# Kernel optimization log

Hardware: AMD Instinct MI355X
Metric: run time of the kernel (lower is better)

Reference implementation:

```python
import jax, jax.numpy as jnp
import numpy as np

B, S, D, H = 4, 2048, 256, 8
SPARSITY = 0.1


def setup_inputs() -> dict:
    key = jax.random.key(0)
    ks = jax.random.split(key, 6)
    s = 0.02
    return {
        "x": jax.random.normal(ks[0], (B, S, D), jnp.float32),
        # nn.MultiheadAttention packed in-projection (W_q;W_k;W_v) and out-projection
        "w_in": jax.random.normal(ks[1], (3 * D, D), jnp.float32) * s,
        "b_in": jnp.zeros((3 * D,), jnp.float32),
        "w_out": jax.random.normal(ks[2], (D, D), jnp.float32) * s,
        "b_out": jnp.zeros((D,), jnp.float32),
        # sparsity gate: Linear(D, D//4) -> ReLU -> Linear(D//4, 1) -> Sigmoid
        "gate_w1": jax.random.normal(ks[3], (D // 4, D), jnp.float32) * s,
        "gate_b1": jnp.zeros((D // 4,), jnp.float32),
        "gate_w2": jax.random.normal(ks[4], (1, D // 4), jnp.float32) * s,
        "gate_b2": jnp.zeros((1,), jnp.float32),
    }


def reference(x, w_in, b_in, w_out, b_out, gate_w1, gate_b1, gate_w2, gate_b2):
    b, s, d = x.shape
    hd = d // H

    # --- adaptive sparse mask (top-k importance gating) ---
    h = jax.nn.relu(jnp.einsum('bsd,fd->bsf', x, gate_w1) + gate_b1)
    importance = jax.nn.sigmoid(jnp.einsum('bsf,of->bso', h, gate_w2) + gate_b2)[..., 0]  # [B,S]
    k = max(1, int(s * SPARSITY))
    _, top_idx = jax.lax.top_k(importance, k)  # [B,k]
    keep = jnp.zeros((b, s), dtype=bool).at[jnp.arange(b)[:, None], top_idx].set(True)  # [B,S]

    # --- multi-head attention with key_padding_mask = ~keep ---
    qkv = jnp.einsum('bsd,ed->bse', x, w_in) + b_in  # [B,S,3D]
    q, kk, v = jnp.split(qkv, 3, axis=-1)
    split_heads = lambda t: t.reshape(b, s, H, hd).transpose(0, 2, 1, 3)  # [B,H,S,hd]
    q, kk, v = split_heads(q), split_heads(kk), split_heads(v)

    scores = jnp.einsum('bhqd,bhkd->bhqk', q, kk) / jnp.sqrt(jnp.asarray(hd, x.dtype))
    neg = jnp.finfo(scores.dtype).min
    scores = jnp.where(keep[:, None, None, :], scores, neg)  # mask non-selected keys
    attn = jax.nn.softmax(scores, axis=-1)

    out = jnp.einsum('bhqk,bhkd->bhqd', attn, v)
    out = out.transpose(0, 2, 1, 3).reshape(b, s, d)
    return jnp.einsum('bsd,od->bso', out, w_out) + b_out
```

## Files before the change

### kernel.cpp

```cpp
#include <hip/hip_runtime.h>
#include <hip/hip_bf16.h>

#define B_  4
#define S_  2048
#define D_  256
#define H_  8
#define HD_ 32
#define K_  204
#define SCALE_ 0.17677669529663687f

#define OFF_IMP    0
#define OFF_KG     8192
#define OFF_VG     217088
#define OFF_FLAGS  425984
#define OFF_KIDX   434176
#define OFF_Q      435200
#define OFF_AO     2532352

typedef __attribute__((ext_vector_type(8))) short short8v;
typedef __attribute__((ext_vector_type(4))) float f32x4;

static __device__ __forceinline__ unsigned short f2bf(float f) {
    unsigned int u = __float_as_uint(f);
    u += 0x7FFFu + ((u >> 16) & 1u);
    return (unsigned short)(u >> 16);
}
static __device__ __forceinline__ float bf2f(unsigned short h) {
    return __uint_as_float((unsigned int)h << 16);
}
static __device__ __forceinline__ short8v pack_bf8(float4 a, float4 b) {
    short8v r;
    r[0]=(short)f2bf(a.x); r[1]=(short)f2bf(a.y); r[2]=(short)f2bf(a.z); r[3]=(short)f2bf(a.w);
    r[4]=(short)f2bf(b.x); r[5]=(short)f2bf(b.y); r[6]=(short)f2bf(b.z); r[7]=(short)f2bf(b.w);
    return r;
}
static __device__ __forceinline__ short8v ld_bf8(const unsigned short* p) {
    union { unsigned int u[4]; short8v v; } cv;
    const uint2 a  = *(const uint2*)(p);
    const uint2 b2 = *(const uint2*)(p + 4);
    cv.u[0] = a.x; cv.u[1] = a.y; cv.u[2] = b2.x; cv.u[3] = b2.y;
    return cv.v;
}
static __device__ __forceinline__ void cvt_store16(
    unsigned short* hi, unsigned short* lo, const float4* v)
{
    #pragma unroll
    for (int q = 0; q < 2; ++q) {
        short8v h, l;
        #pragma unroll
        for (int e = 0; e < 2; ++e) {
            const float4 f = v[q*2 + e];
            const unsigned short h0 = f2bf(f.x), h1 = f2bf(f.y),
                                 h2 = f2bf(f.z), h3 = f2bf(f.w);
            h[e*4+0]=(short)h0; h[e*4+1]=(short)h1; h[e*4+2]=(short)h2; h[e*4+3]=(short)h3;
            l[e*4+0]=(short)f2bf(f.x - bf2f(h0));
            l[e*4+1]=(short)f2bf(f.y - bf2f(h1));
            l[e*4+2]=(short)f2bf(f.z - bf2f(h2));
            l[e*4+3]=(short)f2bf(f.w - bf2f(h3));
        }
        *(short8v*)(hi + q*8) = h;
        *(short8v*)(lo + q*8) = l;
    }
}

__global__ __launch_bounds__(256) void gate_kernel(
    const float* __restrict__ x, const float* __restrict__ gw1,
    const float* __restrict__ gb1, const float* __restrict__ gw2, float* ws)
{
    const int t0 = blockIdx.x * 8;
    const int tid = threadIdx.x;
    __shared__ __align__(16) float xs[8 * D_];
    __shared__ float hred[8 * 64];

    const float4* src = (const float4*)(x + (size_t)t0 * D_);
    ((float4*)xs)[tid]       = src[tid];
    ((float4*)xs)[tid + 256] = src[tid + 256];
    __syncthreads();

    const int c = tid & 3, f = tid >> 2;
    float4 wv[16];
    const float4* wr = (const float4*)(gw1 + (size_t)f * D_) + c;
    #pragma unroll
    for (int j = 0; j < 16; ++j) wv[j] = wr[j * 4];
    const float bb = gb1[f], g2 = gw2[f];

    #pragma unroll
    for (int tk = 0; tk < 8; ++tk) {
        const float4* xr = (const float4*)(xs + tk * D_) + c;
        float a = 0.0f;
        #pragma unroll
        for (int j = 0; j < 16; ++j) {
            float4 xv = xr[j * 4];
            a += wv[j].x*xv.x + wv[j].y*xv.y + wv[j].z*xv.z + wv[j].w*xv.w;
        }
        a += __shfl_xor(a, 1);
        a += __shfl_xor(a, 2);
        if (c == 0) hred[tk * 64 + f] = fmaxf(a + bb, 0.0f) * g2;
    }
    __syncthreads();

    const int tk = tid >> 5, ln = tid & 31;
    float s = hred[tk * 64 + ln] + hred[tk * 64 + ln + 32];
    #pragma unroll
    for (int o = 16; o; o >>= 1) s += __shfl_xor(s, o, 32);
    if (ln == 0) ws[OFF_IMP + t0 + tk] = s;
}

__global__ __launch_bounds__(256) void rank_kernel(const float* __restrict__ ws_imp, int* flags)
{
    const int b  = blockIdx.x >> 7;
    const int ic = blockIdx.x & 127;
    const int tid = threadIdx.x;
    __shared__ __align__(16) float vs[S_];
    const float* src = ws_imp + b * S_;
    #pragma unroll
    for (int cc = 0; cc < S_/(256*4); ++cc)
        ((float4*)vs)[tid + cc*256] = ((const float4*)src)[tid + cc*256];
    __syncthreads();

    const int il = tid >> 4;
    const int c  = tid & 15;
    const int i  = ic * 16 + il;
    const float vi = vs[i];
    int gt = 0, eq = 0;
    const float4* v4 = (const float4*)vs + c * 32;
    #pragma unroll 8
    for (int t = 0; t < 32; ++t) {
        const int j4 = (t + c) & 31;
        float4 w = v4[j4];
        const int base = c * 128 + j4 * 4;
        gt += (w.x > vi); eq += (w.x == vi) && (base + 0 < i);
        gt += (w.y > vi); eq += (w.y == vi) && (base + 1 < i);
        gt += (w.z > vi); eq += (w.z == vi) && (base + 2 < i);
        gt += (w.w > vi); eq += (w.w == vi) && (base + 3 < i);
    }
    int r = gt + eq;
    r += __shfl_xor(r, 1);
    r += __shfl_xor(r, 2);
    r += __shfl_xor(r, 4);
    r += __shfl_xor(r, 8);
    if (c == 0) flags[b * S_ + i] = (r < K_) ? 1 : 0;
}

__global__ __launch_bounds__(256) void emit_kernel(const int* __restrict__ flags, int* kidx)
{
    const int b = blockIdx.x;
    const int t = threadIdx.x;
    __shared__ int fl[S_];
    __shared__ int cs[256];
    const int* src = flags + b * S_;
    #pragma unroll
    for (int c = 0; c < S_/256; ++c) fl[t + c*256] = src[t + c*256];
    __syncthreads();

    int s = 0;
    #pragma unroll
    for (int c = 0; c < 8; ++c) s += fl[t*8 + c];
    cs[t] = s;
    __syncthreads();
    for (int off = 1; off < 256; off <<= 1) {
        int v = (t >= off) ? cs[t - off] : 0;
        __syncthreads();
        cs[t] += v;
        __syncthreads();
    }
    int pos = cs[t] - s;
    #pragma unroll
    for (int c = 0; c < 8; ++c) {
        int idx = t*8 + c;
        if (fl[idx]) { if (pos < K_) kidx[b * K_ + pos] = idx; ++pos; }
    }
}

__global__ __launch_bounds__(256) void kv_kernel(
    const float* __restrict__ x, const float* __restrict__ w_in,
    const float* __restrict__ b_in, float* ws, const int* __restrict__ kidx)
{
    const int b = blockIdx.y, j0 = blockIdx.x * 4, tid = threadIdx.x;
    __shared__ __align__(16) float xs[4 * D_];
    __shared__ int toks[4];
    if (tid < 4) {
        int tk = kidx[b * K_ + j0 + tid];
        toks[tid] = min(max(tk, 0), S_ - 1);
    }
    __syncthreads();
    {
        const int kk = tid >> 6, l = tid & 63;
        ((float4*)xs)[kk * 64 + l] =
            ((const float4*)(x + ((size_t)b * S_ + toks[kk]) * D_))[l];
    }
    __syncthreads();

    const int c = tid & 3, f = tid >> 2;
    #pragma unroll 1
    for (int fg = 0; fg < 8; ++fg) {
        const int eh = fg * 64 + f;
        float4 wv[16];
        const float4* wr = (const float4*)(w_in + (size_t)(D_ + eh) * D_) + c;
        #pragma unroll
        for (int j = 0; j < 16; ++j) wv[j] = wr[j * 4];
        float a0 = 0, a1 = 0, a2 = 0, a3 = 0;
        #pragma unroll
        for (int j = 0; j < 16; ++j) {
            float4 w = wv[j];
            float4 x0 = ((const float4*)(xs + 0*D_))[c + j*4];
            float4 x1 = ((const float4*)(xs + 1*D_))[c + j*4];
            float4 x2 = ((const float4*)(xs + 2*D_))[c + j*4];
            float4 x3 = ((const float4*)(xs + 3*D_))[c + j*4];
            a0 += w.x*x0.x + w.y*x0.y + w.z*x0.z + w.w*x0.w;
            a1 += w.x*x1.x + w.y*x1.y + w.z*x1.z + w.w*x1.w;
            a2 += w.x*x2.x + w.y*x2.y + w.z*x2.z + w.w*x2.w;
            a3 += w.x*x3.x + w.y*x3.y + w.z*x3.z + w.w*x3.w;
        }
        a0 += __shfl_xor(a0, 1); a0 += __shfl_xor(a0, 2);
        a1 += __shfl_xor(a1, 1); a1 += __shfl_xor(a1, 2);
        a2 += __shfl_xor(a2, 1); a2 += __shfl_xor(a2, 2);
        a3 += __shfl_xor(a3, 1); a3 += __shfl_xor(a3, 2);
        if (c == 0) {
            const float bias = b_in[D_ + eh];
            const int isV = eh >> 8;
            const int ee = eh & 255;
            const int h = ee >> 5, d = ee & 31;
            float* dst = ws + (isV ? OFF_VG : OFF_KG) + ((b * H_ + h) * K_) * HD_ + d;
            dst[(j0 + 0) * HD_] = a0 + bias;
            dst[(j0 + 1) * HD_] = a1 + bias;
            dst[(j0 + 2) * HD_] = a2 + bias;
            dst[(j0 + 3) * HD_] = a3 + bias;
        }
    }
}

#define GSTR 80

__global__ __launch_bounds__(256) void gemm_kernel(
    const float* __restrict__ A, const float* __restrict__ W,
    const float* __restrict__ bias, float* __restrict__ C)
{
    __shared__ __align__(16) unsigned short Ash[64 * GSTR];
    __shared__ __align__(16) unsigned short Asl[64 * GSTR];
    __shared__ __align__(16) unsigned short Bsh[64 * GSTR];
    __shared__ __align__(16) unsigned short Bsl[64 * GSTR];

    const int tid = threadIdx.x;
    const int m0 = blockIdx.x * 64, n0 = blockIdx.y * 64;
    const int lane = tid & 63, w = tid >> 6;
    const int c = lane & 15, g = lane >> 4;
    const int mq = w >> 1, nq = w & 1;

    const f32x4 zf = {0.0f, 0.0f, 0.0f, 0.0f};
    f32x4 acc[2][2] = {{zf, zf}, {zf, zf}};

    const int srow = tid >> 2, sseg = tid & 3;
    const float* Ap = A + (size_t)(m0 + srow) * D_ + sseg * 16;
    const float* Wp = W + (size_t)(n0 + srow) * D_ + sseg * 16;

    float4 ar[4], br[4];
    #pragma unroll
    for (int j = 0; j < 4; ++j) { ar[j] = ((const float4*)Ap)[j]; br[j] = ((const float4*)Wp)[j]; }

    for (int k0 = 0; k0 < D_; k0 += 64) {
        __syncthreads();
        cvt_store16(&Ash[srow*GSTR + sseg*16], &Asl[srow*GSTR + sseg*16], ar);
        cvt_store16(&Bsh[srow*GSTR + sseg*16], &Bsl[srow*GSTR + sseg*16], br);
        __syncthreads();
        if (k0 + 64 < D_) {
            #pragma unroll
            for (int j = 0; j < 4; ++j) {
                ar[j] = ((const float4*)(Ap + k0 + 64))[j];
                br[j] = ((const float4*)(Wp + k0 + 64))[j];
            }
        }
        #pragma unroll
        for (int ks = 0; ks < 2; ++ks) {
            short8v am[2][2], bm[2][2];
            #pragma unroll
            for (int t = 0; t < 2; ++t) {
                const int ra = (mq*32 + t*16 + c) * GSTR + ks*32 + g*8;
                am[t][0] = *(const short8v*)&Ash[ra];
                am[t][1] = *(const short8v*)&Asl[ra];
                const int rb = (nq*32 + t*16 + c) * GSTR + ks*32 + g*8;
                bm[t][0] = *(const short8v*)&Bsh[rb];
                bm[t][1] = *(const short8v*)&Bsl[rb];
            }
            #pragma unroll
            for (int mt = 0; mt < 2; ++mt)
                #pragma unroll
                for (int nt = 0; nt < 2; ++nt) {
                    acc[mt][nt] = __builtin_amdgcn_mfma_f32_16x16x32_bf16(am[mt][0], bm[nt][0], acc[mt][nt], 0, 0, 0);
                    acc[mt][nt] = __builtin_amdgcn_mfma_f32_16x16x32_bf16(am[mt][0], bm[nt][1], acc[mt][nt], 0, 0, 0);
                    acc[mt][nt] = __builtin_amdgcn_mfma_f32_16x16x32_bf16(am[mt][1], bm[nt][0], acc[mt][nt], 0, 0, 0);
                }
        }
    }
    #pragma unroll
    for (int nt = 0; nt < 2; ++nt) {
        const int n = n0 + nq*32 + nt*16 + c;
        const float bv = bias[n];
        #pragma unroll
        for (int mt = 0; mt < 2; ++mt) {
            const int m = m0 + mq*32 + mt*16 + g*4;
            #pragma unroll
            for (int r = 0; r < 4; ++r)
                C[(size_t)(m + r) * D_ + n] = acc[mt][nt][r] + bv;
        }
    }
}

#define PSTR 228
#define VSTR 228

__global__ __launch_bounds__(256) void attn_kernel(const float* __restrict__ ws, float* __restrict__ ao)
{
    const int b = blockIdx.z, h = blockIdx.y, q0 = blockIdx.x * 32;
    const int tid = threadIdx.x;
    const int lane = tid & 63, w = tid >> 6;
    const int c = lane & 15, g = lane >> 4;

    __shared__ __align__(16) unsigned short Pl[32 * PSTR];
    __shared__ __align__(16) unsigned short VTl[32 * VSTR];
    __shared__ float redl[4 * 32];
    __shared__ float invl[32];

    const float* KGb = ws + OFF_KG + (size_t)(b * H_ + h) * K_ * HD_;
    const float* VGb = ws + OFF_VG + (size_t)(b * H_ + h) * K_ * HD_;

    for (int i = tid; i < K_ * 8; i += 256) {
        const int j = i >> 3, dc = i & 7;
        const float4 v = ((const float4*)VGb)[i];
        VTl[(dc*4+0)*VSTR + j] = f2bf(v.x);
        VTl[(dc*4+1)*VSTR + j] = f2bf(v.y);
        VTl[(dc*4+2)*VSTR + j] = f2bf(v.z);
        VTl[(dc*4+3)*VSTR + j] = f2bf(v.w);
    }
    {
        const int q = tid >> 3, cc = tid & 7;
        *(unsigned int*)&Pl[q * PSTR + 208 + cc * 2] = 0u;
    }
    for (int i = tid; i < 32 * 20; i += 256) {
        VTl[(i / 20) * VSTR + 204 + (i % 20)] = 0;
    }

    short8v qa[2];
    #pragma unroll
    for (int qt = 0; qt < 2; ++qt) {
        const float* qp = ws + OFF_Q + (size_t)(b * S_ + q0 + qt*16 + c) * D_ + h * HD_ + g * 8;
        qa[qt] = pack_bf8(*(const float4*)qp, *(const float4*)(qp + 4));
    }
    const int njt = (w == 0) ? 4 : 3;
    f32x4 acc[2][4];
    const f32x4 zf = {0.0f, 0.0f, 0.0f, 0.0f};
    #pragma unroll
    for (int qt = 0; qt < 2; ++qt)
        #pragma unroll
        for (int t = 0; t < 4; ++t) acc[qt][t] = zf;

    for (int t = 0; t < njt; ++t) {
        const int jt = w + 4 * t;
        const int jc = min(jt * 16 + c, K_ - 1);
        const float* kp = KGb + (size_t)jc * HD_ + g * 8;
        const short8v kb = pack_bf8(*(const float4*)kp, *(const float4*)(kp + 4));
        acc[0][t] = __builtin_amdgcn_mfma_f32_16x16x32_bf16(qa[0], kb, acc[0][t], 0, 0, 0);
        acc[1][t] = __builtin_amdgcn_mfma_f32_16x16x32_bf16(qa[1], kb, acc[1][t], 0, 0, 0);
    }

    float rs[2][4] = {{0,0,0,0},{0,0,0,0}};
    for (int t = 0; t < njt; ++t) {
        const int jg = (w + 4 * t) * 16 + c;
        const bool val = (jg < K_);
        #pragma unroll
        for (int qt = 0; qt < 2; ++qt) {
            #pragma unroll
            for (int r = 0; r < 4; ++r) {
                const float e = val ? __expf(acc[qt][t][r] * SCALE_) : 0.0f;
                rs[qt][r] += e;
                Pl[(qt*16 + g*4 + r) * PSTR + jg] = f2bf(e);
            }
        }
    }
    #pragma unroll
    for (int qt = 0; qt < 2; ++qt)
        #pragma unroll
        for (int r = 0; r < 4; ++r) {
            float s = rs[qt][r];
            s += __shfl_xor(s, 1); s += __shfl_xor(s, 2);
            s += __shfl_xor(s, 4); s += __shfl_xor(s, 8);
            if (c == 0) redl[w * 32 + qt*16 + g*4 + r] = s;
        }

    __syncthreads();
    if (tid < 32)
        invl[tid] = 1.0f / (redl[tid] + redl[32 + tid] + redl[64 + tid] + redl[96 + tid]);
    __syncthreads();

    const int dt = w >> 1, qt2 = w & 1;
    f32x4 o = zf;
    const unsigned short* vb = &VTl[(dt*16 + c) * VSTR];
    const unsigned short* pb = &Pl[(qt2*16 + c) * PSTR];
    #pragma unroll
    for (int kt = 0; kt < 7; ++kt) {
        const short8v av = ld_bf8(vb + kt*32 + g*8);
        const short8v bv = ld_bf8(pb + kt*32 + g*8);
        o = __builtin_amdgcn_mfma_f32_16x16x32_bf16(av, bv, o, 0, 0, 0);
    }
    const float iv = invl[qt2*16 + c];
    float4 r4; r4.x = o[0]*iv; r4.y = o[1]*iv; r4.z = o[2]*iv; r4.w = o[3]*iv;
    *(float4*)(ao + (size_t)(b * S_ + q0 + qt2*16 + c) * D_ + h * HD_ + dt*16 + g*4) = r4;
}

extern "C" void kernel_launch(void* const* d_in, const int* in_sizes, int n_in,
                              void* d_out, int out_size, void* d_ws, size_t ws_size,
                              hipStream_t stream)
{
    const float* x     = (const float*)d_in[0];
    const float* w_in  = (const float*)d_in[1];
    const float* b_in  = (const float*)d_in[2];
    const float* w_out = (const float*)d_in[3];
    const float* b_out = (const float*)d_in[4];
    const float* gw1   = (const float*)d_in[5];
    const float* gb1   = (const float*)d_in[6];
    const float* gw2   = (const float*)d_in[7];

    float* ws = (float*)d_ws;
    int* flags = (int*)(ws + OFF_FLAGS);
    int* kidx  = (int*)(ws + OFF_KIDX);
    float* out = (float*)d_out;

    gate_kernel<<<B_ * S_ / 8, 256, 0, stream>>>(x, gw1, gb1, gw2, ws);
    rank_kernel<<<B_ * 128, 256, 0, stream>>>(ws + OFF_IMP, flags);
    emit_kernel<<<B_, 256, 0, stream>>>(flags, kidx);
    kv_kernel<<<dim3(51, B_), 256, 0, stream>>>(x, w_in, b_in, ws, kidx);
    gemm_kernel<<<dim3(B_ * S_ / 64, D_ / 64), 256, 0, stream>>>(x, w_in, b_in, ws + OFF_Q);
    attn_kernel<<<dim3(S_ / 32, H_, B_), 256, 0, stream>>>(ws, ws + OFF_AO);
    gemm_kernel<<<dim3(B_ * S_ / 64, D_ / 64), 256, 0, stream>>>(ws + OFF_AO, w_out, b_out, out);
}
```

Before: 167.3 us.

## Fuse all stages into a persistent megakernel with grid-wide barriers

Replaces the seven separate launches with one persistent kernel of 512 blocks. Each block walks virtual tiles of every stage (gate, Q projection, rank, K/V gather projection, attention, output projection), and atomic-counter grid barriers separate the dependent stages, with shared memory reused through a union. The separate emit/prefix-scan pass is dropped: rank now appends selected indices through an atomic counter, so key order is nondeterministic. The goal is to remove per-launch gaps and to overlap the gate and Q GEMM, at the cost of spin-barrier overhead and a deadlock risk if all 512 blocks are not co-resident.

```diff
diff --git a/kernel.cpp b/kernel.cpp
--- a/kernel.cpp
+++ b/kernel.cpp
@@ -12,10 +12,14 @@
 #define OFF_IMP    0
 #define OFF_KG     8192
 #define OFF_VG     217088
-#define OFF_FLAGS  425984
+#define OFF_META   425984
 #define OFF_KIDX   434176
 #define OFF_Q      435200
 #define OFF_AO     2532352
+
+#define GSTR 80
+#define PSTR 228
+#define VSTR 228
 
 typedef __attribute__((ext_vector_type(8))) short short8v;
 typedef __attribute__((ext_vector_type(4))) float f32x4;
@@ -63,14 +67,44 @@
     }
 }
 
-__global__ __launch_bounds__(256) void gate_kernel(
-    const float* __restrict__ x, const float* __restrict__ gw1,
-    const float* __restrict__ gb1, const float* __restrict__ gw2, float* ws)
-{
-    const int t0 = blockIdx.x * 8;
+struct SharedU {
+    union {
+        struct { float xs[8 * D_]; float hred[8 * 64]; } g;
+        struct { float vs[S_]; } r;
+        struct { float xs[4 * D_]; int toks[4]; } k;
+        struct { unsigned short Ash[64*GSTR]; unsigned short Asl[64*GSTR];
+                 unsigned short Bsh[64*GSTR]; unsigned short Bsl[64*GSTR]; } m;
+        struct { unsigned short Pl[32*PSTR]; unsigned short VTl[32*VSTR];
+                 float redl[4*32]; float invl[32]; } a;
+    };
+};
+
+static __device__ __forceinline__ void grid_barrier(int* meta, int target)
+{
+    __syncthreads();
+    if (threadIdx.x == 0) {
+        __threadfence();
+        if (atomicAdd(&meta[0], 1) == (int)gridDim.x - 1) {
+            atomicExch(&meta[0], 0);
+            __threadfence();
+            atomicAdd(&meta[1], 1);
+        } else {
+            while (atomicAdd(&meta[1], 0) < target) __builtin_amdgcn_s_sleep(2);
+        }
+        __threadfence();
+    }
+    __syncthreads();
+}
+
+static __device__ __forceinline__ void gate_tile(
+    SharedU& sh, const float* __restrict__ x, const float* __restrict__ gw1,
+    const float* __restrict__ gb1, const float* __restrict__ gw2, float* ws, int vt)
+{
+    const int t0 = vt * 8;
     const int tid = threadIdx.x;
-    __shared__ __align__(16) float xs[8 * D_];
-    __shared__ float hred[8 * 64];
+    float* xs = sh.g.xs;
+    float* hred = sh.g.hred;
+    __syncthreads();
 
     const float4* src = (const float4*)(x + (size_t)t0 * D_);
     ((float4*)xs)[tid]       = src[tid];
@@ -106,15 +140,17 @@
     if (ln == 0) ws[OFF_IMP + t0 + tk] = s;
 }
 
-__global__ __launch_bounds__(256) void rank_kernel(const float* __restrict__ ws_imp, int* flags)
-{
-    const int b  = blockIdx.x >> 7;
-    const int ic = blockIdx.x & 127;
+static __device__ __forceinline__ void rank_tile(
+    SharedU& sh, const float* __restrict__ imp, int* kidx, int* meta, int vt)
+{
+    const int b  = vt >> 7;
+    const int ic = vt & 127;
     const int tid = threadIdx.x;
-    __shared__ __align__(16) float vs[S_];
-    const float* src = ws_imp + b * S_;
-    #pragma unroll
-    for (int cc = 0; cc < S_/(256*4); ++cc)
+    float* vs = sh.r.vs;
+    __syncthreads();
+    const float* src = imp + b * S_;
+    #pragma unroll
+    for (int cc = 0; cc < 2; ++cc)
         ((float4*)vs)[tid + cc*256] = ((const float4*)src)[tid + cc*256];
     __syncthreads();
 
@@ -139,46 +175,21 @@
     r += __shfl_xor(r, 2);
     r += __shfl_xor(r, 4);
     r += __shfl_xor(r, 8);
-    if (c == 0) flags[b * S_ + i] = (r < K_) ? 1 : 0;
-}
-
-__global__ __launch_bounds__(256) void emit_kernel(const int* __restrict__ flags, int* kidx)
-{
-    const int b = blockIdx.x;
-    const int t = threadIdx.x;
-    __shared__ int fl[S_];
-    __shared__ int cs[256];
-    const int* src = flags + b * S_;
-    #pragma unroll
-    for (int c = 0; c < S_/256; ++c) fl[t + c*256] = src[t + c*256];
-    __syncthreads();
-
-    int s = 0;
-    #pragma unroll
-    for (int c = 0; c < 8; ++c) s += fl[t*8 + c];
-    cs[t] = s;
-    __syncthreads();
-    for (int off = 1; off < 256; off <<= 1) {
-        int v = (t >= off) ? cs[t - off] : 0;
-        __syncthreads();
-        cs[t] += v;
-        __syncthreads();
-    }
-    int pos = cs[t] - s;
-    #pragma unroll
-    for (int c = 0; c < 8; ++c) {
-        int idx = t*8 + c;
-        if (fl[idx]) { if (pos < K_) kidx[b * K_ + pos] = idx; ++pos; }
-    }
-}
-
-__global__ __launch_bounds__(256) void kv_kernel(
-    const float* __restrict__ x, const float* __restrict__ w_in,
-    const float* __restrict__ b_in, float* ws, const int* __restrict__ kidx)
-{
-    const int b = blockIdx.y, j0 = blockIdx.x * 4, tid = threadIdx.x;
-    __shared__ __align__(16) float xs[4 * D_];
-    __shared__ int toks[4];
+    if (c == 0 && r < K_) {
+        const int p = atomicAdd(&meta[2 + b], 1);
+        kidx[b * K_ + p] = i;
+    }
+    __syncthreads();
+}
+
+static __device__ __forceinline__ void kv_tile(
+    SharedU& sh, const float* __restrict__ x, const float* __restrict__ w_in,
+    const float* __restrict__ b_in, float* ws, const int* __restrict__ kidx, int vt)
+{
+    const int b = vt / 51, j0 = (vt % 51) * 4, tid = threadIdx.x;
+    float* xs = sh.k.xs;
+    int* toks = sh.k.toks;
+    __syncthreads();
     if (tid < 4) {
         int tk = kidx[b * K_ + j0 + tid];
         toks[tid] = min(max(tk, 0), S_ - 1);
@@ -228,21 +239,15 @@
             dst[(j0 + 3) * HD_] = a3 + bias;
         }
     }
-}
-
-#define GSTR 80
-
-__global__ __launch_bounds__(256) void gemm_kernel(
-    const float* __restrict__ A, const float* __restrict__ W,
-    const float* __restrict__ bias, float* __restrict__ C)
-{
-    __shared__ __align__(16) unsigned short Ash[64 * GSTR];
-    __shared__ __align__(16) unsigned short Asl[64 * GSTR];
-    __shared__ __align__(16) unsigned short Bsh[64 * GSTR];
-    __shared__ __align__(16) unsigned short Bsl[64 * GSTR];
-
+    __syncthreads();
+}
+
+static __device__ __forceinline__ void gemm_tile(
+    SharedU& sh, const float* __restrict__ A, const float* __restrict__ W,
+    const float* __restrict__ bias, float* __restrict__ C, int vt)
+{
     const int tid = threadIdx.x;
-    const int m0 = blockIdx.x * 64, n0 = blockIdx.y * 64;
+    const int m0 = (vt & 127) * 64, n0 = (vt >> 7) * 64;
     const int lane = tid & 63, w = tid >> 6;
     const int c = lane & 15, g = lane >> 4;
     const int mq = w >> 1, nq = w & 1;
@@ -260,8 +265,8 @@
 
     for (int k0 = 0; k0 < D_; k0 += 64) {
         __syncthreads();
-        cvt_store16(&Ash[srow*GSTR + sseg*16], &Asl[srow*GSTR + sseg*16], ar);
-        cvt_store16(&Bsh[srow*GSTR + sseg*16], &Bsl[srow*GSTR + sseg*16], br);
+        cvt_store16(&sh.m.Ash[srow*GSTR + sseg*16], &sh.m.Asl[srow*GSTR + sseg*16], ar);
+        cvt_store16(&sh.m.Bsh[srow*GSTR + sseg*16], &sh.m.Bsl[srow*GSTR + sseg*16], br);
         __syncthreads();
         if (k0 + 64 < D_) {
             #pragma unroll
@@ -276,11 +281,11 @@
             #pragma unroll
             for (int t = 0; t < 2; ++t) {
                 const int ra = (mq*32 + t*16 + c) * GSTR + ks*32 + g*8;
-                am[t][0] = *(const short8v*)&Ash[ra];
-                am[t][1] = *(const short8v*)&Asl[ra];
+                am[t][0] = *(const short8v*)&sh.m.Ash[ra];
+                am[t][1] = *(const short8v*)&sh.m.Asl[ra];
                 const int rb = (nq*32 + t*16 + c) * GSTR + ks*32 + g*8;
-                bm[t][0] = *(const short8v*)&Bsh[rb];
-                bm[t][1] = *(const short8v*)&Bsl[rb];
+                bm[t][0] = *(const short8v*)&sh.m.Bsh[rb];
+                bm[t][1] = *(const short8v*)&sh.m.Bsl[rb];
             }
             #pragma unroll
             for (int mt = 0; mt < 2; ++mt)
@@ -304,22 +309,23 @@
                 C[(size_t)(m + r) * D_ + n] = acc[mt][nt][r] + bv;
         }
     }
-}
-
-#define PSTR 228
-#define VSTR 228
-
-__global__ __launch_bounds__(256) void attn_kernel(const float* __restrict__ ws, float* __restrict__ ao)
-{
-    const int b = blockIdx.z, h = blockIdx.y, q0 = blockIdx.x * 32;
+    __syncthreads();
+}
+
+static __device__ __forceinline__ void attn_tile(
+    SharedU& sh, const float* __restrict__ ws, float* __restrict__ ao, int vt)
+{
+    const int b = vt >> 9, h = (vt >> 6) & 7, q0 = (vt & 63) * 32;
     const int tid = threadIdx.x;
     const int lane = tid & 63, w = tid >> 6;
     const int c = lane & 15, g = lane >> 4;
 
-    __shared__ __align__(16) unsigned short Pl[32 * PSTR];
-    __shared__ __align__(16) unsigned short VTl[32 * VSTR];
-    __shared__ float redl[4 * 32];
-    __shared__ float invl[32];
+    unsigned short* Pl  = sh.a.Pl;
+    unsigned short* VTl = sh.a.VTl;
+    float* redl = sh.a.redl;
+    float* invl = sh.a.invl;
+
+    __syncthreads();
 
     const float* KGb = ws + OFF_KG + (size_t)(b * H_ + h) * K_ * HD_;
     const float* VGb = ws + OFF_VG + (size_t)(b * H_ + h) * K_ * HD_;
@@ -405,6 +411,40 @@
     const float iv = invl[qt2*16 + c];
     float4 r4; r4.x = o[0]*iv; r4.y = o[1]*iv; r4.z = o[2]*iv; r4.w = o[3]*iv;
     *(float4*)(ao + (size_t)(b * S_ + q0 + qt2*16 + c) * D_ + h * HD_ + dt*16 + g*4) = r4;
+    __syncthreads();
+}
+
+__global__ void init_kernel(int* meta)
+{
+    if (threadIdx.x < 8) meta[threadIdx.x] = 0;
+}
+
+__global__ __launch_bounds__(256, 2) void mega_kernel(
+    const float* __restrict__ x, const float* __restrict__ w_in,
+    const float* __restrict__ b_in, const float* __restrict__ w_out,
+    const float* __restrict__ b_out, const float* __restrict__ gw1,
+    const float* __restrict__ gb1, const float* __restrict__ gw2,
+    float* __restrict__ ws, float* __restrict__ out)
+{
+    __shared__ __align__(16) SharedU sh;
+    int* meta = (int*)(ws + OFF_META);
+    int* kidx = (int*)(ws + OFF_KIDX);
+    const int bid = blockIdx.x, nb = gridDim.x;
+
+    for (int vt = bid; vt < 1024; vt += nb) gate_tile(sh, x, gw1, gb1, gw2, ws, vt);
+    for (int vt = bid; vt < 512; vt += nb) gemm_tile(sh, x, w_in, b_in, ws + OFF_Q, vt);
+    grid_barrier(meta, 1);
+
+    for (int vt = bid; vt < 512; vt += nb) rank_tile(sh, ws + OFF_IMP, kidx, meta, vt);
+    grid_barrier(meta, 2);
+
+    for (int vt = bid; vt < 204; vt += nb) kv_tile(sh, x, w_in, b_in, ws, kidx, vt);
+    grid_barrier(meta, 3);
+
+    for (int vt = bid; vt < 2048; vt += nb) attn_tile(sh, ws, ws + OFF_AO, vt);
+    grid_barrier(meta, 4);
+
+    for (int vt = bid; vt < 512; vt += nb) gemm_tile(sh, ws + OFF_AO, w_out, b_out, out, vt);
 }
 
 extern "C" void kernel_launch(void* const* d_in, const int* in_sizes, int n_in,
@@ -421,15 +461,10 @@
     const float* gw2   = (const float*)d_in[7];
 
     float* ws = (float*)d_ws;
-    int* flags = (int*)(ws + OFF_FLAGS);
-    int* kidx  = (int*)(ws + OFF_KIDX);
+    int* meta = (int*)(ws + OFF_META);
     float* out = (float*)d_out;
 
-    gate_kernel<<<B_ * S_ / 8, 256, 0, stream>>>(x, gw1, gb1, gw2, ws);
-    rank_kernel<<<B_ * 128, 256, 0, stream>>>(ws + OFF_IMP, flags);
-    emit_kernel<<<B_, 256, 0, stream>>>(flags, kidx);
-    kv_kernel<<<dim3(51, B_), 256, 0, stream>>>(x, w_in, b_in, ws, kidx);
-    gemm_kernel<<<dim3(B_ * S_ / 64, D_ / 64), 256, 0, stream>>>(x, w_in, b_in, ws + OFF_Q);
-    attn_kernel<<<dim3(S_ / 32, H_, B_), 256, 0, stream>>>(ws, ws + OFF_AO);
-    gemm_kernel<<<dim3(B_ * S_ / 64, D_ / 64), 256, 0, stream>>>(ws + OFF_AO, w_out, b_out, out);
-}
+    init_kernel<<<1, 64, 0, stream>>>(meta);
+    mega_kernel<<<512, 256, 0, stream>>>(x, w_in, b_in, w_out, b_out,
+                                         gw1, gb1, gw2, ws, out);
+}
```

After: 360.4 us. +115.4%, slower.

## Pre-split operands to bf16 hi/lo once, store K/V/Q in bf16, drop emit kernel

Applied to the files above, without the earlier changes.

The gate kernel now also splits x, w_in and w_out into bf16 hi/lo pairs and writes them to the workspace, so the GEMMs load pre-converted bf16 instead of converting fp32 per tile. K/V and Q are stored as bf16, and the attention output is written as a hi/lo pair, which lowers memory traffic and removes conversion work in the attention kernel. The emit kernel is replaced by atomicAdd compaction inside the rank kernel, saving one launch. That makes key order nondeterministic, which is harmless for the masked softmax. The extra split stores in gate_kernel add write traffic.

```diff
diff --git a/kernel.cpp b/kernel.cpp
--- a/kernel.cpp
+++ b/kernel.cpp
@@ -11,14 +11,26 @@
 
 #define OFF_IMP    0
 #define OFF_KG     8192
-#define OFF_VG     217088
-#define OFF_FLAGS  425984
-#define OFF_KIDX   434176
-#define OFF_Q      435200
-#define OFF_AO     2532352
+#define OFF_VG     112640
+#define OFF_META   217088
+#define OFF_KIDX   217104
+#define OFF_Q      218368
+#define OFF_XH     1266944
+#define OFF_XL     2315520
+#define OFF_AOH    3364096
+#define OFF_AOL    4412672
+#define OFF_WQH    5461248
+#define OFF_WQL    5494016
+#define OFF_WOH    5526784
+#define OFF_WOL    5559552
+
+#define GSTR 80
+#define PSTR 228
+#define VSTR 228
 
 typedef __attribute__((ext_vector_type(8))) short short8v;
 typedef __attribute__((ext_vector_type(4))) float f32x4;
+typedef unsigned short ushort_t;
 
 static __device__ __forceinline__ unsigned short f2bf(float f) {
     unsigned int u = __float_as_uint(f);
@@ -27,12 +39,6 @@
 }
 static __device__ __forceinline__ float bf2f(unsigned short h) {
     return __uint_as_float((unsigned int)h << 16);
-}
-static __device__ __forceinline__ short8v pack_bf8(float4 a, float4 b) {
-    short8v r;
-    r[0]=(short)f2bf(a.x); r[1]=(short)f2bf(a.y); r[2]=(short)f2bf(a.z); r[3]=(short)f2bf(a.w);
-    r[4]=(short)f2bf(b.x); r[5]=(short)f2bf(b.y); r[6]=(short)f2bf(b.z); r[7]=(short)f2bf(b.w);
-    return r;
 }
 static __device__ __forceinline__ short8v ld_bf8(const unsigned short* p) {
     union { unsigned int u[4]; short8v v; } cv;
@@ -41,31 +47,25 @@
     cv.u[0] = a.x; cv.u[1] = a.y; cv.u[2] = b2.x; cv.u[3] = b2.y;
     return cv.v;
 }
-static __device__ __forceinline__ void cvt_store16(
-    unsigned short* hi, unsigned short* lo, const float4* v)
-{
-    #pragma unroll
-    for (int q = 0; q < 2; ++q) {
-        short8v h, l;
-        #pragma unroll
-        for (int e = 0; e < 2; ++e) {
-            const float4 f = v[q*2 + e];
-            const unsigned short h0 = f2bf(f.x), h1 = f2bf(f.y),
-                                 h2 = f2bf(f.z), h3 = f2bf(f.w);
-            h[e*4+0]=(short)h0; h[e*4+1]=(short)h1; h[e*4+2]=(short)h2; h[e*4+3]=(short)h3;
-            l[e*4+0]=(short)f2bf(f.x - bf2f(h0));
-            l[e*4+1]=(short)f2bf(f.y - bf2f(h1));
-            l[e*4+2]=(short)f2bf(f.z - bf2f(h2));
-            l[e*4+3]=(short)f2bf(f.w - bf2f(h3));
-        }
-        *(short8v*)(hi + q*8) = h;
-        *(short8v*)(lo + q*8) = l;
-    }
+static __device__ __forceinline__ void split_store8(
+    const float* __restrict__ src, unsigned short* dh, unsigned short* dl)
+{
+    short8v h, l;
+    #pragma unroll
+    for (int e = 0; e < 8; ++e) {
+        const float f = src[e];
+        const unsigned short hh = f2bf(f);
+        h[e] = (short)hh;
+        l[e] = (short)f2bf(f - bf2f(hh));
+    }
+    *(short8v*)dh = h;
+    *(short8v*)dl = l;
 }
 
 __global__ __launch_bounds__(256) void gate_kernel(
     const float* __restrict__ x, const float* __restrict__ gw1,
-    const float* __restrict__ gb1, const float* __restrict__ gw2, float* ws)
+    const float* __restrict__ gb1, const float* __restrict__ gw2,
+    const float* __restrict__ w_in, const float* __restrict__ w_out, float* ws)
 {
     const int t0 = blockIdx.x * 8;
     const int tid = threadIdx.x;
@@ -77,6 +77,25 @@
     ((float4*)xs)[tid + 256] = src[tid + 256];
     __syncthreads();
 
+    {
+        unsigned short* XH = (unsigned short*)(ws + OFF_XH);
+        unsigned short* XL = (unsigned short*)(ws + OFF_XL);
+        split_store8(xs + tid * 8, XH + (size_t)t0 * D_ + tid * 8,
+                                   XL + (size_t)t0 * D_ + tid * 8);
+    }
+    if (blockIdx.x < 64) {
+        const int e0 = blockIdx.x * 2048 + tid * 8;
+        if (e0 < 65536) {
+            split_store8(w_in + e0, (unsigned short*)(ws + OFF_WQH) + e0,
+                                    (unsigned short*)(ws + OFF_WQL) + e0);
+        } else {
+            const int e = e0 - 65536;
+            split_store8(w_out + e, (unsigned short*)(ws + OFF_WOH) + e,
+                                    (unsigned short*)(ws + OFF_WOL) + e);
+        }
+    }
+    if (blockIdx.x == 0 && tid < 8) ((int*)(ws + OFF_META))[tid] = 0;
+
     const int c = tid & 3, f = tid >> 2;
     float4 wv[16];
     const float4* wr = (const float4*)(gw1 + (size_t)f * D_) + c;
@@ -106,7 +125,8 @@
     if (ln == 0) ws[OFF_IMP + t0 + tk] = s;
 }
 
-__global__ __launch_bounds__(256) void rank_kernel(const float* __restrict__ ws_imp, int* flags)
+__global__ __launch_bounds__(256) void rank_kernel(
+    const float* __restrict__ ws_imp, int* kidx, int* meta)
 {
     const int b  = blockIdx.x >> 7;
     const int ic = blockIdx.x & 127;
@@ -114,7 +134,7 @@
     __shared__ __align__(16) float vs[S_];
     const float* src = ws_imp + b * S_;
     #pragma unroll
-    for (int cc = 0; cc < S_/(256*4); ++cc)
+    for (int cc = 0; cc < 2; ++cc)
         ((float4*)vs)[tid + cc*256] = ((const float4*)src)[tid + cc*256];
     __syncthreads();
 
@@ -139,42 +159,16 @@
     r += __shfl_xor(r, 2);
     r += __shfl_xor(r, 4);
     r += __shfl_xor(r, 8);
-    if (c == 0) flags[b * S_ + i] = (r < K_) ? 1 : 0;
-}
-
-__global__ __launch_bounds__(256) void emit_kernel(const int* __restrict__ flags, int* kidx)
-{
-    const int b = blockIdx.x;
-    const int t = threadIdx.x;
-    __shared__ int fl[S_];
-    __shared__ int cs[256];
-    const int* src = flags + b * S_;
-    #pragma unroll
-    for (int c = 0; c < S_/256; ++c) fl[t + c*256] = src[t + c*256];
-    __syncthreads();
-
-    int s = 0;
-    #pragma unroll
-    for (int c = 0; c < 8; ++c) s += fl[t*8 + c];
-    cs[t] = s;
-    __syncthreads();
-    for (int off = 1; off < 256; off <<= 1) {
-        int v = (t >= off) ? cs[t - off] : 0;
-        __syncthreads();
-        cs[t] += v;
-        __syncthreads();
-    }
-    int pos = cs[t] - s;
-    #pragma unroll
-    for (int c = 0; c < 8; ++c) {
-        int idx = t*8 + c;
-        if (fl[idx]) { if (pos < K_) kidx[b * K_ + pos] = idx; ++pos; }
+    if (c == 0 && r < K_) {
+        const int p = atomicAdd(&meta[2 + b], 1);
+        kidx[b * K_ + p] = i;
     }
 }
 
 __global__ __launch_bounds__(256) void kv_kernel(
     const float* __restrict__ x, const float* __restrict__ w_in,
-    const float* __restrict__ b_in, float* ws, const int* __restrict__ kidx)
+    const float* __restrict__ b_in, unsigned short* __restrict__ KG,
+    unsigned short* __restrict__ VG, const int* __restrict__ kidx)
 {
     const int b = blockIdx.y, j0 = blockIdx.x * 4, tid = threadIdx.x;
     __shared__ __align__(16) float xs[4 * D_];
@@ -221,20 +215,21 @@
             const int isV = eh >> 8;
             const int ee = eh & 255;
             const int h = ee >> 5, d = ee & 31;
-            float* dst = ws + (isV ? OFF_VG : OFF_KG) + ((b * H_ + h) * K_) * HD_ + d;
-            dst[(j0 + 0) * HD_] = a0 + bias;
-            dst[(j0 + 1) * HD_] = a1 + bias;
-            dst[(j0 + 2) * HD_] = a2 + bias;
-            dst[(j0 + 3) * HD_] = a3 + bias;
-        }
-    }
-}
-
-#define GSTR 80
-
+            unsigned short* dst = (isV ? VG : KG) + ((b * H_ + h) * K_) * HD_ + d;
+            dst[(j0 + 0) * HD_] = f2bf(a0 + bias);
+            dst[(j0 + 1) * HD_] = f2bf(a1 + bias);
+            dst[(j0 + 2) * HD_] = f2bf(a2 + bias);
+            dst[(j0 + 3) * HD_] = f2bf(a3 + bias);
+        }
+    }
+}
+
+template<bool QOUT>
 __global__ __launch_bounds__(256) void gemm_kernel(
-    const float* __restrict__ A, const float* __restrict__ W,
-    const float* __restrict__ bias, float* __restrict__ C)
+    const unsigned short* __restrict__ Ah, const unsigned short* __restrict__ Al,
+    const unsigned short* __restrict__ Bh, const unsigned short* __restrict__ Bl,
+    const float* __restrict__ bias, float* __restrict__ Cf,
+    unsigned short* __restrict__ Cq)
 {
     __shared__ __align__(16) unsigned short Ash[64 * GSTR];
     __shared__ __align__(16) unsigned short Asl[64 * GSTR];
@@ -251,23 +246,35 @@
     f32x4 acc[2][2] = {{zf, zf}, {zf, zf}};
 
     const int srow = tid >> 2, sseg = tid & 3;
-    const float* Ap = A + (size_t)(m0 + srow) * D_ + sseg * 16;
-    const float* Wp = W + (size_t)(n0 + srow) * D_ + sseg * 16;
-
-    float4 ar[4], br[4];
-    #pragma unroll
-    for (int j = 0; j < 4; ++j) { ar[j] = ((const float4*)Ap)[j]; br[j] = ((const float4*)Wp)[j]; }
+    const unsigned short* Aph = Ah + (size_t)(m0 + srow) * D_ + sseg * 16;
+    const unsigned short* Apl = Al + (size_t)(m0 + srow) * D_ + sseg * 16;
+    const unsigned short* Bph = Bh + (size_t)(n0 + srow) * D_ + sseg * 16;
+    const unsigned short* Bpl = Bl + (size_t)(n0 + srow) * D_ + sseg * 16;
+
+    short8v arh[2], arl[2], brh[2], brl[2];
+    #pragma unroll
+    for (int u = 0; u < 2; ++u) {
+        arh[u] = *(const short8v*)(Aph + u*8); arl[u] = *(const short8v*)(Apl + u*8);
+        brh[u] = *(const short8v*)(Bph + u*8); brl[u] = *(const short8v*)(Bpl + u*8);
+    }
 
     for (int k0 = 0; k0 < D_; k0 += 64) {
         __syncthreads();
-        cvt_store16(&Ash[srow*GSTR + sseg*16], &Asl[srow*GSTR + sseg*16], ar);
-        cvt_store16(&Bsh[srow*GSTR + sseg*16], &Bsl[srow*GSTR + sseg*16], br);
+        #pragma unroll
+        for (int u = 0; u < 2; ++u) {
+            *(short8v*)&Ash[srow*GSTR + sseg*16 + u*8] = arh[u];
+            *(short8v*)&Asl[srow*GSTR + sseg*16 + u*8] = arl[u];
+            *(short8v*)&Bsh[srow*GSTR + sseg*16 + u*8] = brh[u];
+            *(short8v*)&Bsl[srow*GSTR + sseg*16 + u*8] = brl[u];
+        }
         __syncthreads();
         if (k0 + 64 < D_) {
             #pragma unroll
-            for (int j = 0; j < 4; ++j) {
-                ar[j] = ((const float4*)(Ap + k0 + 64))[j];
-                br[j] = ((const float4*)(Wp + k0 + 64))[j];
+            for (int u = 0; u < 2; ++u) {
+                arh[u] = *(const short8v*)(Aph + k0 + 64 + u*8);
+                arl[u] = *(const short8v*)(Apl + k0 + 64 + u*8);
+                brh[u] = *(const short8v*)(Bph + k0 + 64 + u*8);
+                brl[u] = *(const short8v*)(Bpl + k0 + 64 + u*8);
             }
         }
         #pragma unroll
@@ -300,16 +307,19 @@
         for (int mt = 0; mt < 2; ++mt) {
             const int m = m0 + mq*32 + mt*16 + g*4;
             #pragma unroll
-            for (int r = 0; r < 4; ++r)
-                C[(size_t)(m + r) * D_ + n] = acc[mt][nt][r] + bv;
-        }
-    }
-}
-
-#define PSTR 228
-#define VSTR 228
-
-__global__ __launch_bounds__(256) void attn_kernel(const float* __restrict__ ws, float* __restrict__ ao)
+            for (int r = 0; r < 4; ++r) {
+                const float v = acc[mt][nt][r] + bv;
+                if (QOUT) Cq[(size_t)(m + r) * D_ + n] = f2bf(v);
+                else      Cf[(size_t)(m + r) * D_ + n] = v;
+            }
+        }
+    }
+}
+
+__global__ __launch_bounds__(256) void attn_kernel(
+    const unsigned short* __restrict__ KG, const unsigned short* __restrict__ VG,
+    const unsigned short* __restrict__ Qb,
+    unsigned short* __restrict__ aoh, unsigned short* __restrict__ aol)
 {
     const int b = blockIdx.z, h = blockIdx.y, q0 = blockIdx.x * 32;
     const int tid = threadIdx.x;
@@ -321,16 +331,16 @@
     __shared__ float redl[4 * 32];
     __shared__ float invl[32];
 
-    const float* KGb = ws + OFF_KG + (size_t)(b * H_ + h) * K_ * HD_;
-    const float* VGb = ws + OFF_VG + (size_t)(b * H_ + h) * K_ * HD_;
-
-    for (int i = tid; i < K_ * 8; i += 256) {
-        const int j = i >> 3, dc = i & 7;
-        const float4 v = ((const float4*)VGb)[i];
-        VTl[(dc*4+0)*VSTR + j] = f2bf(v.x);
-        VTl[(dc*4+1)*VSTR + j] = f2bf(v.y);
-        VTl[(dc*4+2)*VSTR + j] = f2bf(v.z);
-        VTl[(dc*4+3)*VSTR + j] = f2bf(v.w);
+    const size_t bh = (size_t)(b * H_ + h) * K_ * HD_;
+    const unsigned short* KGb = KG + bh;
+    const unsigned short* VGb = VG + bh;
+
+    for (int i = tid; i < K_ * 4; i += 256) {
+        const int j = i >> 2, dc = i & 3;
+        const short8v v = *(const short8v*)(VGb + i * 8);
+        #pragma unroll
+        for (int r = 0; r < 8; ++r)
+            VTl[(dc*8 + r)*VSTR + j] = (unsigned short)v[r];
     }
     {
         const int q = tid >> 3, cc = tid & 7;
@@ -342,10 +352,9 @@
 
     short8v qa[2];
     #pragma unroll
-    for (int qt = 0; qt < 2; ++qt) {
-        const float* qp = ws + OFF_Q + (size_t)(b * S_ + q0 + qt*16 + c) * D_ + h * HD_ + g * 8;
-        qa[qt] = pack_bf8(*(const float4*)qp, *(const float4*)(qp + 4));
-    }
+    for (int qt = 0; qt < 2; ++qt)
+        qa[qt] = *(const short8v*)(Qb + (size_t)(b * S_ + q0 + qt*16 + c) * D_ + h * HD_ + g * 8);
+
     const int njt = (w == 0) ? 4 : 3;
     f32x4 acc[2][4];
     const f32x4 zf = {0.0f, 0.0f, 0.0f, 0.0f};
@@ -357,8 +366,7 @@
     for (int t = 0; t < njt; ++t) {
         const int jt = w + 4 * t;
         const int jc = min(jt * 16 + c, K_ - 1);
-        const float* kp = KGb + (size_t)jc * HD_ + g * 8;
-        const short8v kb = pack_bf8(*(const float4*)kp, *(const float4*)(kp + 4));
+        const short8v kb = *(const short8v*)(KGb + (size_t)jc * HD_ + g * 8);
         acc[0][t] = __builtin_amdgcn_mfma_f32_16x16x32_bf16(qa[0], kb, acc[0][t], 0, 0, 0);
         acc[1][t] = __builtin_amdgcn_mfma_f32_16x16x32_bf16(qa[1], kb, acc[1][t], 0, 0, 0);
     }
@@ -403,8 +411,17 @@
         o = __builtin_amdgcn_mfma_f32_16x16x32_bf16(av, bv, o, 0, 0, 0);
     }
     const float iv = invl[qt2*16 + c];
-    float4 r4; r4.x = o[0]*iv; r4.y = o[1]*iv; r4.z = o[2]*iv; r4.w = o[3]*iv;
-    *(float4*)(ao + (size_t)(b * S_ + q0 + qt2*16 + c) * D_ + h * HD_ + dt*16 + g*4) = r4;
+    const size_t oidx = (size_t)(b * S_ + q0 + qt2*16 + c) * D_ + h * HD_ + dt*16 + g*4;
+    ushort4 hh, ll;
+    {
+        const float v0 = o[0]*iv, v1 = o[1]*iv, v2 = o[2]*iv, v3 = o[3]*iv;
+        hh.x = f2bf(v0); ll.x = f2bf(v0 - bf2f(hh.x));
+        hh.y = f2bf(v1); ll.y = f2bf(v1 - bf2f(hh.y));
+        hh.z = f2bf(v2); ll.z = f2bf(v2 - bf2f(hh.z));
+        hh.w = f2bf(v3); ll.w = f2bf(v3 - bf2f(hh.w));
+    }
+    *(ushort4*)(aoh + oidx) = hh;
+    *(ushort4*)(aol + oidx) = ll;
 }
 
 extern "C" void kernel_launch(void* const* d_in, const int* in_sizes, int n_in,
@@ -421,15 +438,27 @@
     const float* gw2   = (const float*)d_in[7];
 
     float* ws = (float*)d_ws;
-    int* flags = (int*)(ws + OFF_FLAGS);
-    int* kidx  = (int*)(ws + OFF_KIDX);
+    int* meta = (int*)(ws + OFF_META);
+    int* kidx = (int*)(ws + OFF_KIDX);
+    unsigned short* KG  = (unsigned short*)(ws + OFF_KG);
+    unsigned short* VG  = (unsigned short*)(ws + OFF_VG);
+    unsigned short* Qb  = (unsigned short*)(ws + OFF_Q);
+    unsigned short* XH  = (unsigned short*)(ws + OFF_XH);
+    unsigned short* XL  = (unsigned short*)(ws + OFF_XL);
+    unsigned short* AOH = (unsigned short*)(ws + OFF_AOH);
+    unsigned short* AOL = (unsigned short*)(ws + OFF_AOL);
+    unsigned short* WQH = (unsigned short*)(ws + OFF_WQH);
+    unsigned short* WQL = (unsigned short*)(ws + OFF_WQL);
+    unsigned short* WOH = (unsigned short*)(ws + OFF_WOH);
+    unsigned short* WOL = (unsigned short*)(ws + OFF_WOL);
     float* out = (float*)d_out;
 
-    gate_kernel<<<B_ * S_ / 8, 256, 0, stream>>>(x, gw1, gb1, gw2, ws);
-    rank_kernel<<<B_ * 128, 256, 0, stream>>>(ws + OFF_IMP, flags);
-    emit_kernel<<<B_, 256, 0, stream>>>(flags, kidx);
-    kv_kernel<<<dim3(51, B_), 256, 0, stream>>>(x, w_in, b_in, ws, kidx);
-    gemm_kernel<<<dim3(B_ * S_ / 64, D_ / 64), 256, 0, stream>>>(x, w_in, b_in, ws + OFF_Q);
-    attn_kernel<<<dim3(S_ / 32, H_, B_), 256, 0, stream>>>(ws, ws + OFF_AO);
-    gemm_kernel<<<dim3(B_ * S_ / 64, D_ / 64), 256, 0, stream>>>(ws + OFF_AO, w_out, b_out, out);
-}
+    gate_kernel<<<B_ * S_ / 8, 256, 0, stream>>>(x, gw1, gb1, gw2, w_in, w_out, ws);
+    rank_kernel<<<B_ * 128, 256, 0, stream>>>(ws + OFF_IMP, kidx, meta);
+    kv_kernel<<<dim3(51, B_), 256, 0, stream>>>(x, w_in, b_in, KG, VG, kidx);
+    gemm_kernel<true><<<dim3(B_ * S_ / 64, D_ / 64), 256, 0, stream>>>(
+        XH, XL, WQH, WQL, b_in, nullptr, Qb);
+    attn_kernel<<<dim3(S_ / 32, H_, B_), 256, 0, stream>>>(KG, VG, Qb, AOH, AOL);
+    gemm_kernel<false><<<dim3(B_ * S_ / 64, D_ / 64), 256, 0, stream>>>(
+        AOH, AOL, WOH, WOL, b_out, out, nullptr);
+}
```

New measurement: 163.6 us. 2.2% less time.
